# Kernel tuning notes

Measured on AMD Instinct MI355X. Metric: run time of the kernel, lower is better.

The kernel has to match this reference:

```python
import jax, jax.numpy as jnp
import numpy as np


def setup_inputs() -> dict:
    key = jax.random.key(0)
    kK, kV, kQ = jax.random.split(key, 3)
    B, D, S = 4, 64, 4096
    K = jax.random.normal(kK, (B, D, S), dtype=jnp.float32)
    V = jax.random.normal(kV, (B, D, S), dtype=jnp.float32)
    Q = jax.random.normal(kQ, (B, D, S), dtype=jnp.float32)
    return {"K": K, "V": V, "Q": Q}


def reference(K, V, Q):
    # K,V: [B, D, Sk], Q: [B, D, Sq]
    d = Q.shape[1]
    # A[b,k,q] = sum_d K[b,d,k] * Q[b,d,q] / sqrt(d)
    A = jnp.einsum("bdk,bdq->bkq", K, Q) / jnp.sqrt(jnp.asarray(d, Q.dtype))
    A = jax.nn.softmax(A, axis=1)  # normalize over keys (dim 1), matching F.softmax(A, 1)
    # R[b,d,q] = sum_k V[b,d,k] * A[b,k,q]
    R = jnp.einsum("bdk,bkq->bdq", V, A)
    return jnp.concatenate((R, Q), axis=1)  # [B, 2D, Sq]
```

## Files before the change

kernel.cpp:

```cpp
#include <hip/hip_runtime.h>
#include <hip/hip_bf16.h>

#define S_LEN 4096
#define D_DIM 64
#define QB 128
#define KB 32
#define NT (S_LEN / KB)
#define TILE_E 4096

typedef __attribute__((ext_vector_type(8)))  short bf16x8;
typedef __attribute__((ext_vector_type(16))) float f32x16;
typedef unsigned int u32;

#define Z16 {0.f,0.f,0.f,0.f,0.f,0.f,0.f,0.f,0.f,0.f,0.f,0.f,0.f,0.f,0.f,0.f}

union bpack8 { __hip_bfloat16 h[8]; bf16x8 v; };
union ppack  { u32 w[4]; bf16x8 v; };
union bload4 { uint2 u; __hip_bfloat16 h[4]; };

static __device__ __forceinline__ float fexp2(float x) {
    return __builtin_amdgcn_exp2f(x);
}
static __device__ __forceinline__ u32 cvtpk(float lo, float hi) {
    u32 r;
    asm("v_cvt_pk_bf16_f32 %0, %1, %2" : "=v"(r) : "v"(lo), "v"(hi));
    return r;
}
static __device__ __forceinline__ void plswap(u32 &a, u32 &b) {
    asm("v_permlane32_swap_b32 %0, %1" : "+v"(a), "+v"(b));
}

#define GLD16(gp, lp) __builtin_amdgcn_global_load_lds( \
    (const __attribute__((address_space(1))) u32*)(const void*)(gp), \
    (__attribute__((address_space(3))) u32*)(void*)(lp), 16, 0, 0)

#define QSCALE 0.18033688011112042f

__global__ __launch_bounds__(256)
void prep_all(const float* __restrict__ K, const float* __restrict__ V,
              const float* __restrict__ Q,
              __hip_bfloat16* __restrict__ KVbf, __hip_bfloat16* __restrict__ Qbf,
              float* __restrict__ out)
{
    const int b = blockIdx.y, x = blockIdx.x, z = blockIdx.z;
    const int t = threadIdx.x;

    if (z == 0) {
        const int key = t & 31, dg = t >> 5;
        const float* src = K + ((size_t)b * D_DIM + dg * 8) * S_LEN + x * KB + key;
        bpack8 u;
        #pragma unroll
        for (int e = 0; e < 8; ++e)
            u.h[e] = __float2bfloat16(src[(size_t)e * S_LEN]);
        *(bf16x8*)&KVbf[((size_t)b * NT + x) * TILE_E + t * 8] = u.v;
    } else if (z == 1) {
        const int kg = t >> 6, d = t & 63;
        const float* p = V + ((size_t)b * D_DIM + d) * S_LEN + x * KB + kg * 8;
        float4 a = *(const float4*)p, c = *(const float4*)(p + 4);
        bpack8 u;
        u.h[0] = __float2bfloat16(a.x); u.h[1] = __float2bfloat16(a.y);
        u.h[2] = __float2bfloat16(a.z); u.h[3] = __float2bfloat16(a.w);
        u.h[4] = __float2bfloat16(c.x); u.h[5] = __float2bfloat16(c.y);
        u.h[6] = __float2bfloat16(c.z); u.h[7] = __float2bfloat16(c.w);
        *(bf16x8*)&KVbf[((size_t)b * NT + x) * TILE_E + 2048 + t * 8] = u.v;
    } else {
        const int q = x * 32 + (t & 31), dg = t >> 5;
        const float* src = Q + ((size_t)b * D_DIM + dg * 8) * S_LEN + q;
        float r[8];
        #pragma unroll
        for (int e = 0; e < 8; ++e) r[e] = src[(size_t)e * S_LEN];
        float* o = out + ((size_t)b * 2 * D_DIM + D_DIM + dg * 8) * S_LEN + q;
        #pragma unroll
        for (int e = 0; e < 8; ++e) o[(size_t)e * S_LEN] = r[e];
        bpack8 u;
        #pragma unroll
        for (int e = 0; e < 8; ++e) u.h[e] = __float2bfloat16(r[e] * QSCALE);
        *(bf16x8*)&Qbf[((size_t)b * S_LEN + q) * D_DIM + dg * 8] = u.v;
    }
}

__global__ __launch_bounds__(256, 4)
void attn_fwd(const __hip_bfloat16* __restrict__ KVbf,
              const __hip_bfloat16* __restrict__ Qbf,
              float* __restrict__ out,
              __hip_bfloat16* __restrict__ accPb, float* __restrict__ lP,
              int ntiles, int nb, int direct)
{
    const int b  = blockIdx.y;
    const int z  = blockIdx.z;
    const int q0 = blockIdx.x * QB;

    const int t    = threadIdx.x;
    const int lane = t & 63;
    const int w    = t >> 6;
    const int l5   = lane & 31;
    const int h    = lane >> 5;

    __shared__ __align__(16) char Ls[2][16384];

    const __hip_bfloat16* kvb = KVbf + ((size_t)b * NT + z * ntiles) * TILE_E;

    const __hip_bfloat16* qrow = Qbf + ((size_t)b * S_LEN + q0 + w * 32 + l5) * D_DIM;
    bf16x8 qf[4];
    #pragma unroll
    for (int j = 0; j < 4; ++j)
        qf[j] = *(const bf16x8*)&qrow[(2 * j + h) * 8];

    #pragma unroll
    for (int sub = 0; sub < 2; ++sub) {
        GLD16(kvb + sub * TILE_E + t * 8,        Ls[0] + sub * 8192 + w * 1024);
        GLD16(kvb + sub * TILE_E + 2048 + t * 8, Ls[0] + sub * 8192 + 4096 + w * 1024);
    }
    __syncthreads();

    float lsum = 0.f;
    f32x16 acc[2] = {Z16, Z16};
    int cur = 0;

    const int npairs = ntiles >> 1;
    for (int p = 0; p < npairs; ++p) {
        if (p + 1 < npairs) {
            const __hip_bfloat16* nx = kvb + (size_t)(2 * p + 2) * TILE_E;
            #pragma unroll
            for (int sub = 0; sub < 2; ++sub) {
                GLD16(nx + sub * TILE_E + t * 8,
                      Ls[cur ^ 1] + sub * 8192 + w * 1024);
                GLD16(nx + sub * TILE_E + 2048 + t * 8,
                      Ls[cur ^ 1] + sub * 8192 + 4096 + w * 1024);
            }
        }

        #pragma unroll
        for (int sub = 0; sub < 2; ++sub) {
            const char* Lk = Ls[cur] + sub * 8192;
            const char* Lv = Lk + 4096;

            f32x16 s = Z16;
            __builtin_amdgcn_s_setprio(1);
            #pragma unroll
            for (int j = 0; j < 4; ++j) {
                bf16x8 kf = *(const bf16x8*)(Lk + ((2 * j + h) * 32 + l5) * 16);
                s = __builtin_amdgcn_mfma_f32_32x32x16_bf16(kf, qf[j], s, 0, 0, 0);
            }
            __builtin_amdgcn_s_setprio(0);

            #pragma unroll
            for (int r = 0; r < 16; ++r) s[r] = fexp2(s[r]);
            {
                float a0 = (s[0] + s[1])   + (s[2] + s[3]);
                float a1 = (s[4] + s[5])   + (s[6] + s[7]);
                float a2 = (s[8] + s[9])   + (s[10] + s[11]);
                float a3 = (s[12] + s[13]) + (s[14] + s[15]);
                lsum += (a0 + a1) + (a2 + a3);
            }

            u32 A = cvtpk(s[0],  s[1]),  Bw = cvtpk(s[2],  s[3]);
            u32 C = cvtpk(s[4],  s[5]),  Dw = cvtpk(s[6],  s[7]);
            u32 E = cvtpk(s[8],  s[9]),  F  = cvtpk(s[10], s[11]);
            u32 G = cvtpk(s[12], s[13]), H  = cvtpk(s[14], s[15]);
            plswap(A, C); plswap(Bw, Dw); plswap(E, G); plswap(F, H);
            ppack pf[2];
            pf[0].w[0] = A; pf[0].w[1] = Bw; pf[0].w[2] = C; pf[0].w[3] = Dw;
            pf[1].w[0] = E; pf[1].w[1] = F;  pf[1].w[2] = G; pf[1].w[3] = H;

            __builtin_amdgcn_s_setprio(1);
            #pragma unroll
            for (int j = 0; j < 2; ++j)
                #pragma unroll
                for (int dt = 0; dt < 2; ++dt) {
                    bf16x8 vf = *(const bf16x8*)(Lv + ((2 * j + h) * 64 + dt * 32 + l5) * 16);
                    acc[dt] = __builtin_amdgcn_mfma_f32_32x32x16_bf16(vf, pf[j].v, acc[dt], 0, 0, 0);
                }
            __builtin_amdgcn_s_setprio(0);
        }

        __syncthreads();
        cur ^= 1;
    }

    lsum += __shfl_xor(lsum, 32);

    const int qcol = q0 + w * 32 + l5;
    if (!direct) {
        __hip_bfloat16* ap = accPb + (size_t)(z * nb + b) * D_DIM * S_LEN;
        #pragma unroll
        for (int dt = 0; dt < 2; ++dt)
            #pragma unroll
            for (int r = 0; r < 16; ++r) {
                int d = dt * 32 + (r & 3) + 8 * (r >> 2) + 4 * h;
                ap[(size_t)d * S_LEN + qcol] = __float2bfloat16(acc[dt][r]);
            }
        if (h == 0)
            lP[(size_t)(z * nb + b) * S_LEN + qcol] = lsum;
    } else {
        float inv = 1.f / lsum;
        float* op = out + (size_t)b * 2 * D_DIM * S_LEN;
        #pragma unroll
        for (int dt = 0; dt < 2; ++dt)
            #pragma unroll
            for (int r = 0; r < 16; ++r) {
                int d = dt * 32 + (r & 3) + 8 * (r >> 2) + 4 * h;
                op[(size_t)d * S_LEN + qcol] = acc[dt][r] * inv;
            }
    }
}

__global__ __launch_bounds__(256)
void attn_combine(const __hip_bfloat16* __restrict__ accPb,
                  const float* __restrict__ lP,
                  float* __restrict__ out, int nsplit, int nb)
{
    int gid = blockIdx.x * 256 + threadIdx.x;
    int q4   = gid & (S_LEN / 4 - 1);
    int rest = gid >> 10;
    int d    = rest & (D_DIM - 1);
    int b    = rest >> 6;
    if (b >= nb) return;
    size_t qoff = (size_t)q4 * 4;

    float num[4] = {0.f,0.f,0.f,0.f}, den[4] = {0.f,0.f,0.f,0.f};
    for (int z = 0; z < nsplit; ++z) {
        bload4 a;
        a.u = *(const uint2*)&accPb[((size_t)(z * nb + b) * D_DIM + d) * S_LEN + qoff];
        float4 lz = *(const float4*)&lP[(size_t)(z * nb + b) * S_LEN + qoff];
        num[0] += __bfloat162float(a.h[0]); num[1] += __bfloat162float(a.h[1]);
        num[2] += __bfloat162float(a.h[2]); num[3] += __bfloat162float(a.h[3]);
        den[0] += lz.x; den[1] += lz.y; den[2] += lz.z; den[3] += lz.w;
    }
    float4 r;
    r.x = num[0] / den[0]; r.y = num[1] / den[1];
    r.z = num[2] / den[2]; r.w = num[3] / den[3];
    *(float4*)&out[((size_t)b * 2 * D_DIM + d) * S_LEN + qoff] = r;
}

extern "C" void kernel_launch(void* const* d_in, const int* in_sizes, int n_in,
                              void* d_out, int out_size, void* d_ws, size_t ws_size,
                              hipStream_t stream) {
    const float* K = (const float*)d_in[0];
    const float* V = (const float*)d_in[1];
    const float* Q = (const float*)d_in[2];
    float* out = (float*)d_out;

    const int B = in_sizes[0] / (D_DIM * S_LEN);
    const size_t kvE = (size_t)B * NT * TILE_E;
    const size_t qE  = (size_t)B * S_LEN * D_DIM;

    auto need = [&](int ns) -> size_t {
        return (kvE + qE) * 2
             + (size_t)ns * B * D_DIM * S_LEN * 2
             + (size_t)ns * B * S_LEN * 4;
    };
    const int cand[4] = {8, 4, 2, 1};
    int nsplit = 1;
    for (int i = 0; i < 4; ++i)
        if (need(cand[i]) <= ws_size) { nsplit = cand[i]; break; }
    const int direct = (nsplit == 1);

    __hip_bfloat16* KVbf = (__hip_bfloat16*)d_ws;
    __hip_bfloat16* Qbf  = KVbf + kvE;
    __hip_bfloat16* accPb = Qbf + qE;
    float* lP = (float*)(accPb + (size_t)nsplit * B * D_DIM * S_LEN);

    prep_all<<<dim3(NT, B, 3), dim3(256), 0, stream>>>(K, V, Q, KVbf, Qbf, out);

    attn_fwd<<<dim3(S_LEN / QB, B, nsplit), dim3(256), 0, stream>>>(
        KVbf, Qbf, out, accPb, lP, NT / nsplit, B, direct);

    if (!direct) {
        int total = B * D_DIM * (S_LEN / 4);
        attn_combine<<<dim3(total / 256), dim3(256), 0, stream>>>(
            accPb, lP, out, nsplit, B);
    }
}
```

Before: 38.09 us.

## Load K/V fragments directly from global memory instead of LDS double buffering

Result: slower. 41.32 us (+8.5%).

```diff
diff --git a/kernel.cpp b/kernel.cpp
--- a/kernel.cpp
+++ b/kernel.cpp
@@ -29,10 +29,6 @@
 static __device__ __forceinline__ void plswap(u32 &a, u32 &b) {
     asm("v_permlane32_swap_b32 %0, %1" : "+v"(a), "+v"(b));
 }
-
-#define GLD16(gp, lp) __builtin_amdgcn_global_load_lds( \
-    (const __attribute__((address_space(1))) u32*)(const void*)(gp), \
-    (__attribute__((address_space(3))) u32*)(void*)(lp), 16, 0, 0)
 
 #define QSCALE 0.18033688011112042f
 
@@ -96,9 +92,14 @@
     const int l5   = lane & 31;
     const int h    = lane >> 5;
 
-    __shared__ __align__(16) char Ls[2][16384];
-
-    const __hip_bfloat16* kvb = KVbf + ((size_t)b * NT + z * ntiles) * TILE_E;
+    const __hip_bfloat16* kvb = KVbf + ((size_t)b * NT + (size_t)z * ntiles) * TILE_E;
+
+    int kOff[4], vOff[4];
+    #pragma unroll
+    for (int j = 0; j < 4; ++j) {
+        kOff[j] = ((2 * j + h) * 32 + l5) * 8;
+        vOff[j] = 2048 + ((2 * (j >> 1) + h) * 64 + (j & 1) * 32 + l5) * 8;
+    }
 
     const __hip_bfloat16* qrow = Qbf + ((size_t)b * S_LEN + q0 + w * 32 + l5) * D_DIM;
     bf16x8 qf[4];
@@ -106,76 +107,53 @@
     for (int j = 0; j < 4; ++j)
         qf[j] = *(const bf16x8*)&qrow[(2 * j + h) * 8];
 
-    #pragma unroll
-    for (int sub = 0; sub < 2; ++sub) {
-        GLD16(kvb + sub * TILE_E + t * 8,        Ls[0] + sub * 8192 + w * 1024);
-        GLD16(kvb + sub * TILE_E + 2048 + t * 8, Ls[0] + sub * 8192 + 4096 + w * 1024);
-    }
-    __syncthreads();
-
     float lsum = 0.f;
     f32x16 acc[2] = {Z16, Z16};
-    int cur = 0;
-
-    const int npairs = ntiles >> 1;
-    for (int p = 0; p < npairs; ++p) {
-        if (p + 1 < npairs) {
-            const __hip_bfloat16* nx = kvb + (size_t)(2 * p + 2) * TILE_E;
+
+    #pragma unroll 2
+    for (int it = 0; it < ntiles; ++it) {
+        const __hip_bfloat16* tp = kvb + (size_t)it * TILE_E;
+
+        bf16x8 kf[4], vf[4];
+        #pragma unroll
+        for (int j = 0; j < 4; ++j) kf[j] = *(const bf16x8*)&tp[kOff[j]];
+        #pragma unroll
+        for (int j = 0; j < 4; ++j) vf[j] = *(const bf16x8*)&tp[vOff[j]];
+
+        f32x16 s = Z16;
+        __builtin_amdgcn_s_setprio(1);
+        #pragma unroll
+        for (int j = 0; j < 4; ++j)
+            s = __builtin_amdgcn_mfma_f32_32x32x16_bf16(kf[j], qf[j], s, 0, 0, 0);
+        __builtin_amdgcn_s_setprio(0);
+
+        #pragma unroll
+        for (int r = 0; r < 16; ++r) s[r] = fexp2(s[r]);
+        {
+            float a0 = (s[0] + s[1])   + (s[2] + s[3]);
+            float a1 = (s[4] + s[5])   + (s[6] + s[7]);
+            float a2 = (s[8] + s[9])   + (s[10] + s[11]);
+            float a3 = (s[12] + s[13]) + (s[14] + s[15]);
+            lsum += (a0 + a1) + (a2 + a3);
+        }
+
+        u32 A = cvtpk(s[0],  s[1]),  Bw = cvtpk(s[2],  s[3]);
+        u32 C = cvtpk(s[4],  s[5]),  Dw = cvtpk(s[6],  s[7]);
+        u32 E = cvtpk(s[8],  s[9]),  F  = cvtpk(s[10], s[11]);
+        u32 G = cvtpk(s[12], s[13]), H  = cvtpk(s[14], s[15]);
+        plswap(A, C); plswap(Bw, Dw); plswap(E, G); plswap(F, H);
+        ppack pf[2];
+        pf[0].w[0] = A; pf[0].w[1] = Bw; pf[0].w[2] = C; pf[0].w[3] = Dw;
+        pf[1].w[0] = E; pf[1].w[1] = F;  pf[1].w[2] = G; pf[1].w[3] = H;
+
+        __builtin_amdgcn_s_setprio(1);
+        #pragma unroll
+        for (int j = 0; j < 2; ++j)
             #pragma unroll
-            for (int sub = 0; sub < 2; ++sub) {
-                GLD16(nx + sub * TILE_E + t * 8,
-                      Ls[cur ^ 1] + sub * 8192 + w * 1024);
-                GLD16(nx + sub * TILE_E + 2048 + t * 8,
-                      Ls[cur ^ 1] + sub * 8192 + 4096 + w * 1024);
-            }
-        }
-
-        #pragma unroll
-        for (int sub = 0; sub < 2; ++sub) {
-            const char* Lk = Ls[cur] + sub * 8192;
-            const char* Lv = Lk + 4096;
-
-            f32x16 s = Z16;
-            __builtin_amdgcn_s_setprio(1);
-            #pragma unroll
-            for (int j = 0; j < 4; ++j) {
-                bf16x8 kf = *(const bf16x8*)(Lk + ((2 * j + h) * 32 + l5) * 16);
-                s = __builtin_amdgcn_mfma_f32_32x32x16_bf16(kf, qf[j], s, 0, 0, 0);
-            }
-            __builtin_amdgcn_s_setprio(0);
-
-            #pragma unroll
-            for (int r = 0; r < 16; ++r) s[r] = fexp2(s[r]);
-            {
-                float a0 = (s[0] + s[1])   + (s[2] + s[3]);
-                float a1 = (s[4] + s[5])   + (s[6] + s[7]);
-                float a2 = (s[8] + s[9])   + (s[10] + s[11]);
-                float a3 = (s[12] + s[13]) + (s[14] + s[15]);
-                lsum += (a0 + a1) + (a2 + a3);
-            }
-
-            u32 A = cvtpk(s[0],  s[1]),  Bw = cvtpk(s[2],  s[3]);
-            u32 C = cvtpk(s[4],  s[5]),  Dw = cvtpk(s[6],  s[7]);
-            u32 E = cvtpk(s[8],  s[9]),  F  = cvtpk(s[10], s[11]);
-            u32 G = cvtpk(s[12], s[13]), H  = cvtpk(s[14], s[15]);
-            plswap(A, C); plswap(Bw, Dw); plswap(E, G); plswap(F, H);
-            ppack pf[2];
-            pf[0].w[0] = A; pf[0].w[1] = Bw; pf[0].w[2] = C; pf[0].w[3] = Dw;
-            pf[1].w[0] = E; pf[1].w[1] = F;  pf[1].w[2] = G; pf[1].w[3] = H;
-
-            __builtin_amdgcn_s_setprio(1);
-            #pragma unroll
-            for (int j = 0; j < 2; ++j)
-                #pragma unroll
-                for (int dt = 0; dt < 2; ++dt) {
-                    bf16x8 vf = *(const bf16x8*)(Lv + ((2 * j + h) * 64 + dt * 32 + l5) * 16);
-                    acc[dt] = __builtin_amdgcn_mfma_f32_32x32x16_bf16(vf, pf[j].v, acc[dt], 0, 0, 0);
-                }
-            __builtin_amdgcn_s_setprio(0);
-        }
-
-        __syncthreads();
-        cur ^= 1;
+            for (int dt = 0; dt < 2; ++dt)
+                acc[dt] = __builtin_amdgcn_mfma_f32_32x32x16_bf16(
+                    vf[2 * j + dt], pf[j].v, acc[dt], 0, 0, 0);
+        __builtin_amdgcn_s_setprio(0);
     }
 
     lsum += __shfl_xor(lsum, 32);
```

## Process two 32-query tiles per wave to reuse K/V fragments

Applied to the files above, without the earlier changes.

After: 38.31 us. Within noise of the previous version (+0.6%).

```diff
diff --git a/kernel.cpp b/kernel.cpp
--- a/kernel.cpp
+++ b/kernel.cpp
@@ -3,7 +3,7 @@
 
 #define S_LEN 4096
 #define D_DIM 64
-#define QB 128
+#define QB 256
 #define KB 32
 #define NT (S_LEN / KB)
 #define TILE_E 4096
@@ -28,6 +28,26 @@
 }
 static __device__ __forceinline__ void plswap(u32 &a, u32 &b) {
     asm("v_permlane32_swap_b32 %0, %1" : "+v"(a), "+v"(b));
+}
+
+struct pfrag { ppack p0, p1; };
+static __device__ __forceinline__ pfrag packP(const f32x16& s) {
+    u32 A = cvtpk(s[0],  s[1]),  Bw = cvtpk(s[2],  s[3]);
+    u32 C = cvtpk(s[4],  s[5]),  Dw = cvtpk(s[6],  s[7]);
+    u32 E = cvtpk(s[8],  s[9]),  F  = cvtpk(s[10], s[11]);
+    u32 G = cvtpk(s[12], s[13]), H  = cvtpk(s[14], s[15]);
+    plswap(A, C); plswap(Bw, Dw); plswap(E, G); plswap(F, H);
+    pfrag r;
+    r.p0.w[0] = A; r.p0.w[1] = Bw; r.p0.w[2] = C; r.p0.w[3] = Dw;
+    r.p1.w[0] = E; r.p1.w[1] = F;  r.p1.w[2] = G; r.p1.w[3] = H;
+    return r;
+}
+static __device__ __forceinline__ float treesum(const f32x16& s) {
+    float a0 = (s[0] + s[1])   + (s[2] + s[3]);
+    float a1 = (s[4] + s[5])   + (s[6] + s[7]);
+    float a2 = (s[8] + s[9])   + (s[10] + s[11]);
+    float a3 = (s[12] + s[13]) + (s[14] + s[15]);
+    return (a0 + a1) + (a2 + a3);
 }
 
 #define GLD16(gp, lp) __builtin_amdgcn_global_load_lds( \
@@ -79,7 +99,7 @@
     }
 }
 
-__global__ __launch_bounds__(256, 4)
+__global__ __launch_bounds__(256, 2)
 void attn_fwd(const __hip_bfloat16* __restrict__ KVbf,
               const __hip_bfloat16* __restrict__ Qbf,
               float* __restrict__ out,
@@ -98,13 +118,16 @@
 
     __shared__ __align__(16) char Ls[2][16384];
 
-    const __hip_bfloat16* kvb = KVbf + ((size_t)b * NT + z * ntiles) * TILE_E;
-
-    const __hip_bfloat16* qrow = Qbf + ((size_t)b * S_LEN + q0 + w * 32 + l5) * D_DIM;
-    bf16x8 qf[4];
+    const __hip_bfloat16* kvb = KVbf + ((size_t)b * NT + (size_t)z * ntiles) * TILE_E;
+
+    const __hip_bfloat16* qrowA = Qbf + ((size_t)b * S_LEN + q0 + w * 64 + l5) * D_DIM;
+    const __hip_bfloat16* qrowB = qrowA + 32 * D_DIM;
+    bf16x8 qfA[4], qfB[4];
     #pragma unroll
-    for (int j = 0; j < 4; ++j)
-        qf[j] = *(const bf16x8*)&qrow[(2 * j + h) * 8];
+    for (int j = 0; j < 4; ++j) {
+        qfA[j] = *(const bf16x8*)&qrowA[(2 * j + h) * 8];
+        qfB[j] = *(const bf16x8*)&qrowB[(2 * j + h) * 8];
+    }
 
     #pragma unroll
     for (int sub = 0; sub < 2; ++sub) {
@@ -113,8 +136,8 @@
     }
     __syncthreads();
 
-    float lsum = 0.f;
-    f32x16 acc[2] = {Z16, Z16};
+    float lsumA = 0.f, lsumB = 0.f;
+    f32x16 accA[2] = {Z16, Z16}, accB[2] = {Z16, Z16};
     int cur = 0;
 
     const int npairs = ntiles >> 1;
@@ -135,41 +158,46 @@
             const char* Lk = Ls[cur] + sub * 8192;
             const char* Lv = Lk + 4096;
 
-            f32x16 s = Z16;
+            bf16x8 kf[4];
+            #pragma unroll
+            for (int j = 0; j < 4; ++j)
+                kf[j] = *(const bf16x8*)(Lk + ((2 * j + h) * 32 + l5) * 16);
+
+            f32x16 sA = Z16, sB = Z16;
             __builtin_amdgcn_s_setprio(1);
             #pragma unroll
             for (int j = 0; j < 4; ++j) {
-                bf16x8 kf = *(const bf16x8*)(Lk + ((2 * j + h) * 32 + l5) * 16);
-                s = __builtin_amdgcn_mfma_f32_32x32x16_bf16(kf, qf[j], s, 0, 0, 0);
+                sA = __builtin_amdgcn_mfma_f32_32x32x16_bf16(kf[j], qfA[j], sA, 0, 0, 0);
+                sB = __builtin_amdgcn_mfma_f32_32x32x16_bf16(kf[j], qfB[j], sB, 0, 0, 0);
             }
             __builtin_amdgcn_s_setprio(0);
 
-            #pragma unroll
-            for (int r = 0; r < 16; ++r) s[r] = fexp2(s[r]);
-            {
-                float a0 = (s[0] + s[1])   + (s[2] + s[3]);
-                float a1 = (s[4] + s[5])   + (s[6] + s[7]);
-                float a2 = (s[8] + s[9])   + (s[10] + s[11]);
-                float a3 = (s[12] + s[13]) + (s[14] + s[15]);
-                lsum += (a0 + a1) + (a2 + a3);
-            }
-
-            u32 A = cvtpk(s[0],  s[1]),  Bw = cvtpk(s[2],  s[3]);
-            u32 C = cvtpk(s[4],  s[5]),  Dw = cvtpk(s[6],  s[7]);
-            u32 E = cvtpk(s[8],  s[9]),  F  = cvtpk(s[10], s[11]);
-            u32 G = cvtpk(s[12], s[13]), H  = cvtpk(s[14], s[15]);
-            plswap(A, C); plswap(Bw, Dw); plswap(E, G); plswap(F, H);
-            ppack pf[2];
-            pf[0].w[0] = A; pf[0].w[1] = Bw; pf[0].w[2] = C; pf[0].w[3] = Dw;
-            pf[1].w[0] = E; pf[1].w[1] = F;  pf[1].w[2] = G; pf[1].w[3] = H;
+            bf16x8 vf[4];
+            #pragma unroll
+            for (int j = 0; j < 2; ++j)
+                #pragma unroll
+                for (int dt = 0; dt < 2; ++dt)
+                    vf[2 * j + dt] = *(const bf16x8*)(Lv + ((2 * j + h) * 64 + dt * 32 + l5) * 16);
+
+            #pragma unroll
+            for (int r = 0; r < 16; ++r) sA[r] = fexp2(sA[r]);
+            #pragma unroll
+            for (int r = 0; r < 16; ++r) sB[r] = fexp2(sB[r]);
+            lsumA += treesum(sA);
+            lsumB += treesum(sB);
+
+            pfrag pA = packP(sA), pB = packP(sB);
 
             __builtin_amdgcn_s_setprio(1);
             #pragma unroll
             for (int j = 0; j < 2; ++j)
                 #pragma unroll
                 for (int dt = 0; dt < 2; ++dt) {
-                    bf16x8 vf = *(const bf16x8*)(Lv + ((2 * j + h) * 64 + dt * 32 + l5) * 16);
-                    acc[dt] = __builtin_amdgcn_mfma_f32_32x32x16_bf16(vf, pf[j].v, acc[dt], 0, 0, 0);
+                    const bf16x8 vv = vf[2 * j + dt];
+                    const ppack& pa = j ? pA.p1 : pA.p0;
+                    const ppack& pb = j ? pB.p1 : pB.p0;
+                    accA[dt] = __builtin_amdgcn_mfma_f32_32x32x16_bf16(vv, pa.v, accA[dt], 0, 0, 0);
+                    accB[dt] = __builtin_amdgcn_mfma_f32_32x32x16_bf16(vv, pb.v, accB[dt], 0, 0, 0);
                 }
             __builtin_amdgcn_s_setprio(0);
         }
@@ -178,9 +206,10 @@
         cur ^= 1;
     }
 
-    lsum += __shfl_xor(lsum, 32);
-
-    const int qcol = q0 + w * 32 + l5;
+    lsumA += __shfl_xor(lsumA, 32);
+    lsumB += __shfl_xor(lsumB, 32);
+
+    const int qA = q0 + w * 64 + l5;
     if (!direct) {
         __hip_bfloat16* ap = accPb + (size_t)(z * nb + b) * D_DIM * S_LEN;
         #pragma unroll
@@ -188,19 +217,23 @@
             #pragma unroll
             for (int r = 0; r < 16; ++r) {
                 int d = dt * 32 + (r & 3) + 8 * (r >> 2) + 4 * h;
-                ap[(size_t)d * S_LEN + qcol] = __float2bfloat16(acc[dt][r]);
+                ap[(size_t)d * S_LEN + qA]      = __float2bfloat16(accA[dt][r]);
+                ap[(size_t)d * S_LEN + qA + 32] = __float2bfloat16(accB[dt][r]);
             }
-        if (h == 0)
-            lP[(size_t)(z * nb + b) * S_LEN + qcol] = lsum;
+        if (h == 0) {
+            lP[(size_t)(z * nb + b) * S_LEN + qA]      = lsumA;
+            lP[(size_t)(z * nb + b) * S_LEN + qA + 32] = lsumB;
+        }
     } else {
-        float inv = 1.f / lsum;
+        float invA = 1.f / lsumA, invB = 1.f / lsumB;
         float* op = out + (size_t)b * 2 * D_DIM * S_LEN;
         #pragma unroll
         for (int dt = 0; dt < 2; ++dt)
             #pragma unroll
             for (int r = 0; r < 16; ++r) {
                 int d = dt * 32 + (r & 3) + 8 * (r >> 2) + 4 * h;
-                op[(size_t)d * S_LEN + qcol] = acc[dt][r] * inv;
+                op[(size_t)d * S_LEN + qA]      = accA[dt][r] * invA;
+                op[(size_t)d * S_LEN + qA + 32] = accB[dt][r] * invB;
             }
     }
 }
```
